# Performance work log

Measured on AMD Instinct MI355X. Metric: run time of the kernel, lower is better.

## Reference

```python
import jax, jax.numpy as jnp
import numpy as np

ALPHA = 0.2  # LeakyReLU negative slope


def setup_inputs() -> dict:
    key = jax.random.key(0)
    k_h, k_adj, k_a1, k_a2 = jax.random.split(key, 4)
    B, N, D = 8, 2048, 128
    h = jax.random.normal(k_h, (B, N, D), dtype=jnp.float32)
    adj = jax.random.randint(k_adj, (B, N, N), 0, 2, dtype=jnp.int32)
    # attention parameters a1, a2: shape (D, 1) as in the original layer
    a1 = jax.random.normal(k_a1, (D, 1), dtype=jnp.float32) * (1.0 / np.sqrt(D))
    a2 = jax.random.normal(k_a2, (D, 1), dtype=jnp.float32) * (1.0 / np.sqrt(D))
    return {"h": h, "adj": adj, "a1": a1, "a2": a2}


def reference(h, adj, a1, a2):
    # h: [B, N, D]; adj: [B, N, N] (int mask); a1, a2: [D, 1]
    f1 = h @ a1                                  # [B, N, 1] per-source score
    f2 = h @ a2                                  # [B, N, 1] per-target score
    logits = f1 + jnp.swapaxes(f2, 1, 2)         # broadcast -> [B, N, N]
    logits = jnp.where(logits > 0, logits, ALPHA * logits)  # LeakyReLU
    logits = jnp.where(adj > 0, logits, -jnp.inf)            # adjacency mask
    prob = jax.nn.softmax(logits, axis=2)        # [B, N, N]
    h_prime = jnp.einsum('bij,bjd->bid', prob, h)  # weighted aggregation
    return jax.nn.elu(h_prime)                   # concat=True branch
```

## Files before the change

kernel.cpp:

```cpp
#include <hip/hip_runtime.h>
#include <hip/hip_bf16.h>
#include <math.h>

#define BB 8
#define NN 2048
#define DD 128
#define ALPHA 0.2f
#define LOG2E 1.4426950408889634f

typedef __attribute__((ext_vector_type(8))) short short8;
typedef __attribute__((ext_vector_type(4))) float f32x4;

__device__ inline unsigned short bf16_rne(float v) {
    unsigned int x = __float_as_uint(v);
    unsigned int r = x + 0x7FFFu + ((x >> 16) & 1u);
    return (unsigned short)(r >> 16);
}

__device__ __forceinline__ void stage16(const void* gsrc, void* lds) {
    __builtin_amdgcn_global_load_lds(
        (const __attribute__((address_space(1))) unsigned int*)gsrc,
        (__attribute__((address_space(3))) unsigned int*)lds, 16, 0, 0);
}

__global__ __launch_bounds__(256) void bitpack_kernel(const int* __restrict__ adj,
                                                      unsigned* __restrict__ bits) {
    unsigned g0 = blockIdx.x * 256 + threadIdx.x;
#pragma unroll
    for (int rep = 0; rep < 2; ++rep) {
        unsigned g = g0 + rep * 524288u;
        const int4* p = reinterpret_cast<const int4*>(adj + (size_t)g * 32);
        int4 v[8];
#pragma unroll
        for (int i = 0; i < 8; ++i) v[i] = p[i];
        unsigned w = 0;
#pragma unroll
        for (int i = 0; i < 8; ++i) {
            w |= ((unsigned)v[i].x) << (4 * i);
            w |= ((unsigned)v[i].y) << (4 * i + 1);
            w |= ((unsigned)v[i].z) << (4 * i + 2);
            w |= ((unsigned)v[i].w) << (4 * i + 3);
        }
        bits[g] = w;
    }
}

__global__ __launch_bounds__(256) void pack_kernel(const float* __restrict__ h,
                                                   const float* __restrict__ a1,
                                                   const float* __restrict__ a2,
                                                   float* __restrict__ f1,
                                                   float* __restrict__ f2,
                                                   unsigned short* __restrict__ panel) {
    __shared__ float hs[32][DD];
    int blk = blockIdx.x;
    int b   = blk >> 6;
    int ks  = blk & 63;
    int r0  = ks * 32;
    int t   = threadIdx.x;

    const float* hb = h + ((size_t)b * NN + r0) * DD;
#pragma unroll
    for (int m = 0; m < 4; ++m) {
        int off = t * 4 + m * 1024;
        *reinterpret_cast<float4*>(&hs[0][0] + off) =
            *reinterpret_cast<const float4*>(hb + off);
    }
    __syncthreads();

    {
        int row = t >> 3, d0 = (t & 7) * 16;
        float s1 = 0.f, s2 = 0.f;
#pragma unroll
        for (int q = 0; q < 4; ++q) {
            float4 hv  = *reinterpret_cast<const float4*>(&hs[row][d0 + q * 4]);
            float4 av1 = *reinterpret_cast<const float4*>(a1 + d0 + q * 4);
            float4 av2 = *reinterpret_cast<const float4*>(a2 + d0 + q * 4);
            s1 += hv.x * av1.x + hv.y * av1.y + hv.z * av1.z + hv.w * av1.w;
            s2 += hv.x * av2.x + hv.y * av2.y + hv.z * av2.z + hv.w * av2.w;
        }
#pragma unroll
        for (int off = 1; off < 8; off <<= 1) {
            s1 += __shfl_xor(s1, off, 64);
            s2 += __shfl_xor(s2, off, 64);
        }
        if ((t & 7) == 0) {
            f1[b * NN + r0 + row] = s1 * LOG2E;
            f2[b * NN + r0 + row] = s2 * LOG2E;
        }
    }

    {
        int n = t >> 1;
        size_t base = (((size_t)b * 64 + ks) * 128 + n) * 32;
#pragma unroll
        for (int cc = 0; cc < 2; ++cc) {
            int c = (t & 1) * 2 + cc;
            short8 v;
#pragma unroll
            for (int e = 0; e < 8; ++e) v[e] = (short)bf16_rne(hs[c * 8 + e][n]);
            *reinterpret_cast<short8*>(panel + base + (size_t)c * 8) = v;
        }
    }
}

__global__ __launch_bounds__(512, 2) void gat_mfma(const unsigned* __restrict__ bits,
                                                   const float* __restrict__ f1,
                                                   const float* __restrict__ f2,
                                                   const unsigned short* __restrict__ panel,
                                                   float* __restrict__ out) {
    __shared__ __align__(16) unsigned char stg[2][16384];
    __shared__ __align__(16) float red[4][16][132];
    __shared__ float sden[4][2][16];

    int blk  = blockIdx.x;
    int b    = blk & 7;
    int tile = blk >> 3;
    int i0   = tile * 64;
    int t    = threadIdx.x;
    int w    = t >> 6, l = t & 63;
    int lr   = l & 15, lc = l >> 4;
    int mt   = w >> 1, kh = w & 1;

    const unsigned char* pslice = (const unsigned char*)(panel + (size_t)b * (64 * 128 * 32));
    const float* f2b = f2 + b * NN;
    int irow = i0 + mt * 16 + lr;
    float f1r = f1[b * NN + irow];
    const unsigned* brow = bits + ((size_t)(b * NN + irow) << 6);

    f32x4 acc[8];
#pragma unroll
    for (int nt = 0; nt < 8; ++nt) acc[nt] = (f32x4){0.f, 0.f, 0.f, 0.f};
    f32x4 accd = (f32x4){0.f, 0.f, 0.f, 0.f};

    short8 ones;
#pragma unroll
    for (int e = 0; e < 8; ++e) ones[e] = (short)0x3F80;

    int soff = w * 1024 + l * 16;
    int doff = w * 1024;

    stage16(pslice + soff, stg[0] + doff);
    stage16(pslice + 8192 + soff, stg[0] + 8192 + doff);

    unsigned bcur = brow[kh];
    float4 g0c = *reinterpret_cast<const float4*>(f2b + kh * 32 + lc * 8);
    float4 g1c = *reinterpret_cast<const float4*>(f2b + kh * 32 + lc * 8 + 4);

    const unsigned char* myfrag0 = &stg[0][0] + kh * 8192 + lr * 64 + lc * 16;
    const unsigned char* myfrag1 = &stg[1][0] + kh * 8192 + lr * 64 + lc * 16;

#pragma unroll 2
    for (int s = 0; s < 32; ++s) {
        int cur = s & 1;
        __syncthreads();

        if (s < 31) {
            const unsigned char* src = pslice + (size_t)(s + 1) * 16384;
            unsigned char* dst = stg[cur ^ 1];
            stage16(src + soff, dst + doff);
            stage16(src + 8192 + soff, dst + 8192 + doff);
        }

        unsigned bs = bcur >> (lc * 8);
        float4 g0 = g0c, g1 = g1c;
        if (s < 31) {
            int cn = 2 * (s + 1) + kh;
            bcur = brow[cn];
            g0c = *reinterpret_cast<const float4*>(f2b + cn * 32 + lc * 8);
            g1c = *reinterpret_cast<const float4*>(f2b + cn * 32 + lc * 8 + 4);
        }

        float f2v[8] = {g0.x, g0.y, g0.z, g0.w, g1.x, g1.y, g1.z, g1.w};
        float wv[8];
#pragma unroll
        for (int e = 0; e < 8; ++e) {
            float x  = f1r + f2v[e];
            float ee = fmaxf(x, ALPHA * x);
            float gv = __builtin_amdgcn_exp2f(ee);
            wv[e] = ((bs >> e) & 1u) ? gv : 0.f;
        }
        union { short8 s8; __hip_bfloat162 h2[4]; } u;
#pragma unroll
        for (int p = 0; p < 4; ++p)
            u.h2[p] = __float22bfloat162_rn(make_float2(wv[2 * p], wv[2 * p + 1]));

        const unsigned char* frag = cur ? myfrag1 : myfrag0;
#pragma unroll
        for (int nt = 0; nt < 8; ++nt) {
            short8 bfv = *reinterpret_cast<const short8*>(frag + nt * 1024);
            acc[nt] = __builtin_amdgcn_mfma_f32_16x16x32_bf16(u.s8, bfv, acc[nt], 0, 0, 0);
        }
        accd = __builtin_amdgcn_mfma_f32_16x16x32_bf16(u.s8, ones, accd, 0, 0, 0);
    }

    if (lr == 0) {
#pragma unroll
        for (int r = 0; r < 4; ++r) sden[mt][kh][lc * 4 + r] = accd[r];
    }

    if (kh == 0) {
#pragma unroll
        for (int nt = 0; nt < 8; ++nt) {
            float* p = &red[mt][lc * 4][nt * 16 + lr];
#pragma unroll
            for (int r = 0; r < 4; ++r) p[r * 132] = acc[nt][r];
        }
    }
    __syncthreads();
    if (kh == 1) {
#pragma unroll
        for (int nt = 0; nt < 8; ++nt) {
            float* p = &red[mt][lc * 4][nt * 16 + lr];
#pragma unroll
            for (int r = 0; r < 4; ++r) p[r * 132] += acc[nt][r];
        }
    }
    __syncthreads();

    {
        int row = t >> 3, col0 = (t & 7) * 16;
        int rmt = row >> 4, rloc = row & 15;
        float den = sden[rmt][0][rloc] + sden[rmt][1][rloc];
        float inv = 1.0f / den;
        float* ob = out + ((size_t)b * NN + i0 + row) * DD;
#pragma unroll
        for (int q = 0; q < 4; ++q) {
            int col = col0 + q * 4;
            float4 v = *reinterpret_cast<const float4*>(&red[rmt][rloc][col]);
            float r0 = v.x * inv, r1 = v.y * inv, r2 = v.z * inv, r3 = v.w * inv;
            r0 = (r0 > 0.f) ? r0 : expm1f(r0);
            r1 = (r1 > 0.f) ? r1 : expm1f(r1);
            r2 = (r2 > 0.f) ? r2 : expm1f(r2);
            r3 = (r3 > 0.f) ? r3 : expm1f(r3);
            *reinterpret_cast<float4*>(ob + col) = make_float4(r0, r1, r2, r3);
        }
    }
}

extern "C" void kernel_launch(void* const* d_in, const int* in_sizes, int n_in,
                              void* d_out, int out_size, void* d_ws, size_t ws_size,
                              hipStream_t stream) {
    const float* h   = (const float*)d_in[0];
    const int*   adj = (const int*)d_in[1];
    const float* a1  = (const float*)d_in[2];
    const float* a2  = (const float*)d_in[3];
    float* out = (float*)d_out;

    float* f1 = (float*)d_ws;
    float* f2 = f1 + BB * NN;
    unsigned short* panel = (unsigned short*)(f2 + BB * NN);
    unsigned* bits = (unsigned*)(panel + (size_t)BB * 64 * 128 * 32);

    bitpack_kernel<<<2048, 256, 0, stream>>>(adj, bits);
    pack_kernel<<<BB * 64, 256, 0, stream>>>(h, a1, a2, f1, f2, panel);
    gat_mfma<<<BB * 32, 512, 0, stream>>>(bits, f1, f2, panel, out);
}
```

Before: 241.4 us.

## Pre-swizzle h panel into MFMA fragment order and halve row tile per block

The packed bf16 panel of h is now written in the exact lane order the MFMA B-fragment reads, so each lane loads a contiguous 16-byte chunk (l*16) from LDS instead of a strided lr*64+lc*16 pattern. The pack kernel's shared tile is padded to 132 columns to avoid bank conflicts during the transpose. The attention kernel goes from 512-thread blocks over 64 rows to 256-thread blocks over 32 rows, doubling the grid to 512 blocks to fill more CUs. The trade-off is that each staged panel is reused by fewer rows, so global/L2 panel traffic doubles.

```diff
diff --git a/kernel.cpp b/kernel.cpp
--- a/kernel.cpp
+++ b/kernel.cpp
@@ -51,18 +51,19 @@
                                                    float* __restrict__ f1,
                                                    float* __restrict__ f2,
                                                    unsigned short* __restrict__ panel) {
-    __shared__ float hs[32][DD];
+    __shared__ float hs[32][132];
     int blk = blockIdx.x;
     int b   = blk >> 6;
-    int ks  = blk & 63;
-    int r0  = ks * 32;
+    int c   = blk & 63;
+    int r0  = c * 32;
     int t   = threadIdx.x;
 
     const float* hb = h + ((size_t)b * NN + r0) * DD;
 #pragma unroll
     for (int m = 0; m < 4; ++m) {
-        int off = t * 4 + m * 1024;
-        *reinterpret_cast<float4*>(&hs[0][0] + off) =
+        int off = m * 1024 + t * 4;
+        int row = off >> 7, col = off & 127;
+        *reinterpret_cast<float4*>(&hs[row][col]) =
             *reinterpret_cast<const float4*>(hb + off);
     }
     __syncthreads();
@@ -90,38 +91,42 @@
     }
 
     {
-        int n = t >> 1;
-        size_t base = (((size_t)b * 64 + ks) * 128 + n) * 32;
-#pragma unroll
-        for (int cc = 0; cc < 2; ++cc) {
-            int c = (t & 1) * 2 + cc;
-            short8 v;
-#pragma unroll
-            for (int e = 0; e < 8; ++e) v[e] = (short)bf16_rne(hs[c * 8 + e][n]);
-            *reinterpret_cast<short8*>(panel + base + (size_t)c * 8) = v;
-        }
-    }
-}
-
-__global__ __launch_bounds__(512, 2) void gat_mfma(const unsigned* __restrict__ bits,
+        int nt = t >> 5;
+        int l0 = (t & 31) * 2;
+        int rg = l0 >> 4;
+        int col = nt * 16 + (l0 & 15);
+        short8 v0, v1;
+#pragma unroll
+        for (int e = 0; e < 8; ++e) {
+            float2 v = *reinterpret_cast<const float2*>(&hs[rg * 8 + e][col]);
+            v0[e] = (short)bf16_rne(v.x);
+            v1[e] = (short)bf16_rne(v.y);
+        }
+        unsigned short* dst = panel + ((size_t)(b * 64 + c) * 4096) + nt * 512 + l0 * 8;
+        *reinterpret_cast<short8*>(dst)     = v0;
+        *reinterpret_cast<short8*>(dst + 8) = v1;
+    }
+}
+
+__global__ __launch_bounds__(256, 2) void gat_mfma(const unsigned* __restrict__ bits,
                                                    const float* __restrict__ f1,
                                                    const float* __restrict__ f2,
                                                    const unsigned short* __restrict__ panel,
                                                    float* __restrict__ out) {
     __shared__ __align__(16) unsigned char stg[2][16384];
-    __shared__ __align__(16) float red[4][16][132];
-    __shared__ float sden[4][2][16];
+    __shared__ __align__(16) float red[2][16][132];
+    __shared__ float sden[2][2][16];
 
     int blk  = blockIdx.x;
     int b    = blk & 7;
     int tile = blk >> 3;
-    int i0   = tile * 64;
+    int i0   = tile * 32;
     int t    = threadIdx.x;
     int w    = t >> 6, l = t & 63;
     int lr   = l & 15, lc = l >> 4;
     int mt   = w >> 1, kh = w & 1;
 
-    const unsigned char* pslice = (const unsigned char*)(panel + (size_t)b * (64 * 128 * 32));
+    const unsigned char* pslice = (const unsigned char*)(panel + (size_t)b * (64 * 4096));
     const float* f2b = f2 + b * NN;
     int irow = i0 + mt * 16 + lr;
     float f1r = f1[b * NN + irow];
@@ -136,18 +141,16 @@
 #pragma unroll
     for (int e = 0; e < 8; ++e) ones[e] = (short)0x3F80;
 
-    int soff = w * 1024 + l * 16;
-    int doff = w * 1024;
-
-    stage16(pslice + soff, stg[0] + doff);
-    stage16(pslice + 8192 + soff, stg[0] + 8192 + doff);
+    int soff = w * 4096 + l * 16;
+    int doff = w * 4096;
+
+#pragma unroll
+    for (int r = 0; r < 4; ++r)
+        stage16(pslice + soff + r * 1024, &stg[0][0] + doff + r * 1024);
 
     unsigned bcur = brow[kh];
     float4 g0c = *reinterpret_cast<const float4*>(f2b + kh * 32 + lc * 8);
     float4 g1c = *reinterpret_cast<const float4*>(f2b + kh * 32 + lc * 8 + 4);
-
-    const unsigned char* myfrag0 = &stg[0][0] + kh * 8192 + lr * 64 + lc * 16;
-    const unsigned char* myfrag1 = &stg[1][0] + kh * 8192 + lr * 64 + lc * 16;
 
 #pragma unroll 2
     for (int s = 0; s < 32; ++s) {
@@ -156,9 +159,10 @@
 
         if (s < 31) {
             const unsigned char* src = pslice + (size_t)(s + 1) * 16384;
-            unsigned char* dst = stg[cur ^ 1];
-            stage16(src + soff, dst + doff);
-            stage16(src + 8192 + soff, dst + 8192 + doff);
+            unsigned char* dst = &stg[cur ^ 1][0];
+#pragma unroll
+            for (int r = 0; r < 4; ++r)
+                stage16(src + soff + r * 1024, dst + doff + r * 1024);
         }
 
         unsigned bs = bcur >> (lc * 8);
@@ -184,7 +188,7 @@
         for (int p = 0; p < 4; ++p)
             u.h2[p] = __float22bfloat162_rn(make_float2(wv[2 * p], wv[2 * p + 1]));
 
-        const unsigned char* frag = cur ? myfrag1 : myfrag0;
+        const unsigned char* frag = &stg[cur][0] + kh * 8192 + l * 16;
 #pragma unroll
         for (int nt = 0; nt < 8; ++nt) {
             short8 bfv = *reinterpret_cast<const short8*>(frag + nt * 1024);
@@ -249,9 +253,9 @@
     float* f1 = (float*)d_ws;
     float* f2 = f1 + BB * NN;
     unsigned short* panel = (unsigned short*)(f2 + BB * NN);
-    unsigned* bits = (unsigned*)(panel + (size_t)BB * 64 * 128 * 32);
+    unsigned* bits = (unsigned*)(panel + (size_t)BB * 64 * 4096);
 
     bitpack_kernel<<<2048, 256, 0, stream>>>(adj, bits);
     pack_kernel<<<BB * 64, 256, 0, stream>>>(h, a1, a2, f1, f2, panel);
-    gat_mfma<<<BB * 32, 512, 0, stream>>>(bits, f1, f2, panel, out);
-}
+    gat_mfma<<<BB * 64, 256, 0, stream>>>(bits, f1, f2, panel, out);
+}
```

After: 244.1 us. About the same (+1.1%).
